# Optimization experiments

Measured on AMD Instinct MI355X. Metric: run time of the kernel, lower is better.

The kernel has to match this reference:

```python
import jax, jax.numpy as jnp
import numpy as np

N_BASIS = 8
CUTOFF = 5.0
NORM_FACTOR = 16.0


def setup_inputs() -> dict:
    key = jax.random.key(0)
    ks = jax.random.split(key, 10)
    N, E, C = 20000, 320000, 32
    s = 1.0 / np.sqrt(C)
    return {
        "node0": jax.random.normal(ks[0], (N, C), jnp.float32),
        "node1": jax.random.normal(ks[1], (N, C, 3), jnp.float32),
        "node2": jax.random.normal(ks[2], (N, C, 3, 3), jnp.float32),
        "rij": jax.random.normal(ks[3], (E, 3), jnp.float32) * 1.5,
        "Wrad": jax.random.normal(ks[4], (11, N_BASIS, C), jnp.float32) * 0.3,
        "U": jax.random.normal(ks[5], (3, C, C), jnp.float32) * s,
        "V": jax.random.normal(ks[6], (8, C, C), jnp.float32) * s,
        "Wg": jax.random.normal(ks[7], (3, C, C), jnp.float32) * s,
        "idx_i": jax.random.randint(ks[8], (E,), 0, N),
        "idx_j": jax.random.randint(ks[9], (E,), 0, N),
    }


def reference(node0, node1, node2, rij, Wrad, U, V, Wg, idx_i, idx_j):
    N, C = node0.shape
    # radial basis (Gaussian RBF * cosine cutoff envelope)
    dist = jnp.sqrt(jnp.sum(rij * rij, -1) + 1e-12)           # [E]
    rhat = rij / dist[:, None]                                 # [E,3]
    centers = jnp.linspace(0.5, CUTOFF, N_BASIS, dtype=node0.dtype)
    fc = 0.5 * (jnp.cos(jnp.pi * jnp.clip(dist / CUTOFF, 0.0, 1.0)) + 1.0)
    rbf = jnp.exp(-4.0 * (dist[:, None] - centers) ** 2) * fc[:, None]  # [E,B]
    # per-coupling-path radial filters: 11 paths (in_way, r_way, out_way)
    w = jnp.einsum('eb,pbc->pec', rbf, Wrad)                   # [11,E,C]
    # gather neighbor (node_j) features per edge
    g0 = node0[idx_j]                                          # [E,C]
    g1 = node1[idx_j]                                          # [E,C,3]
    g2 = node2[idx_j]                                          # [E,C,3,3]
    m1 = rhat                                                  # [E,3]
    m2 = rhat[:, :, None] * rhat[:, None, :]                   # [E,3,3]
    # graph conv: contract node_j tensor with r-way moment, weighted by radial filter
    # paths: 0:(0,0,0) 1:(0,1,1) 2:(0,2,2) 3:(1,0,1) 4:(1,1,0) 5:(1,1,2)
    #        6:(1,2,1) 7:(2,0,2) 8:(2,1,1) 9:(2,2,0) 10:(2,2,2)
    msg0 = (g0 * w[0]
            + jnp.einsum('eca,ea->ec', g1, m1) * w[4]
            + jnp.einsum('ecab,eab->ec', g2, m2) * w[9])
    msg1 = (jnp.einsum('ec,ea->eca', g0 * w[1], m1)
            + g1 * w[3][:, :, None]
            + jnp.einsum('eca,eab->ecb', g1, m2) * w[6][:, :, None]
            + jnp.einsum('ecab,eb->eca', g2, m1) * w[8][:, :, None])
    msg2 = (jnp.einsum('ec,eab->ecab', g0 * w[2], m2)
            + jnp.einsum('eca,eb->ecab', g1 * w[5][:, :, None], m1)
            + g2 * w[7][:, :, None, None]
            + jnp.einsum('ecab,ebd->ecad', g2, m2) * w[10][:, :, None, None])
    # scatter_add aggregation into per-atom features, normalized
    a0 = jax.ops.segment_sum(msg0, idx_i, num_segments=N) / NORM_FACTOR
    a1 = jax.ops.segment_sum(msg1, idx_i, num_segments=N) / NORM_FACTOR
    a2 = jax.ops.segment_sum(msg2, idx_i, num_segments=N) / NORM_FACTOR
    # multi-body self-interaction (2-body linear U + 3-body products V)
    y0 = (jnp.einsum('nc,cd->nd', a0, U[0])
          + jnp.einsum('nc,cd->nd', a0 * a0, V[0])
          + jnp.einsum('nc,cd->nd', jnp.einsum('nca,nca->nc', a1, a1), V[3])
          + jnp.einsum('nc,cd->nd', jnp.einsum('ncab,ncab->nc', a2, a2), V[6]))
    y1 = (jnp.einsum('nca,cd->nda', a1, U[1])
          + jnp.einsum('nca,cd->nda', a0[:, :, None] * a1, V[1])
          + jnp.einsum('nca,cd->nda', jnp.einsum('nca,ncab->ncb', a1, a2), V[5]))
    y2 = (jnp.einsum('ncab,cd->ndab', a2, U[2])
          + jnp.einsum('ncab,cd->ndab', a0[:, :, None, None] * a2, V[2])
          + jnp.einsum('ncab,cd->ndab', a1[:, :, :, None] * a1[:, :, None, :], V[4])
          + jnp.einsum('ncab,cd->ndab', jnp.einsum('ncab,ncbd->ncad', a2, a2), V[7]))
    # gated nonlinearity (scalar channel gates tensor ways) + residual add
    new0 = node0 + jax.nn.silu(y0 @ Wg[0])
    new1 = node1 + y1 * jax.nn.silu(y0 @ Wg[1])[:, :, None]
    new2 = node2 + y2 * jax.nn.silu(y0 @ Wg[2])[:, :, None, None]
    return (new0, new1, new2)
```

## Files before the change

kernel.cpp:

```cpp
#include <hip/hip_runtime.h>
#include <hip/hip_fp16.h>

#define NCH 32
#define NB 8
#define NPB 8

typedef __attribute__((ext_vector_type(2))) _Float16 half2r;

__device__ __forceinline__ unsigned short f2h(float f) {
    return __half_as_ushort(__float2half_rn(f));
}
__device__ __forceinline__ float h2f_lo(unsigned int u) {
    half2r v = __builtin_bit_cast(half2r, u);
    return (float)v.x;
}
__device__ __forceinline__ float h2f_hi(unsigned int u) {
    half2r v = __builtin_bit_cast(half2r, u);
    return (float)v.y;
}
__device__ __forceinline__ unsigned int pack2h(float lo, float hi) {
    return (unsigned int)f2h(lo) | ((unsigned int)f2h(hi) << 16);
}

__device__ __forceinline__ float fdot2u(unsigned int a, unsigned int b, float c) {
#if __has_builtin(__builtin_amdgcn_fdot2)
    return __builtin_amdgcn_fdot2(__builtin_bit_cast(half2r, a),
                                  __builtin_bit_cast(half2r, b), c, false);
#else
    half2r av = __builtin_bit_cast(half2r, a);
    half2r bv = __builtin_bit_cast(half2r, b);
    return c + (float)av.x * (float)bv.x + (float)av.y * (float)bv.y;
#endif
}

__device__ __forceinline__ void acc8h(float& y, uint4 w, uint4 f) {
    y = fdot2u(w.x, f.x, y);
    y = fdot2u(w.y, f.y, y);
    y = fdot2u(w.z, f.z, y);
    y = fdot2u(w.w, f.w, y);
}
__device__ __forceinline__ void acc8fh(float& y, uint4 w, float4 a, float4 b) {
    y += h2f_lo(w.x) * a.x + h2f_hi(w.x) * a.y + h2f_lo(w.y) * a.z + h2f_hi(w.y) * a.w
       + h2f_lo(w.z) * b.x + h2f_hi(w.z) * b.y + h2f_lo(w.w) * b.z + h2f_hi(w.w) * b.w;
}

__global__ __launch_bounds__(256) void wprep_kernel(
    const float* __restrict__ U, const float* __restrict__ V,
    const float* __restrict__ Wg, unsigned short* __restrict__ wswz)
{
    int idx = blockIdx.x * 256 + threadIdx.x;
    if (idx >= 14 * 1024) return;
    int m = idx >> 10, r = idx & 1023;
    int c = r >> 5, d = r & 31;
    float v;
    if (m < 3)       v = U[m * 1024 + c * 32 + d];
    else if (m < 11) v = V[(m - 3) * 1024 + c * 32 + d];
    else             v = Wg[(m - 11) * 1024 + c * 32 + d];
    wswz[m * 1024 + (c >> 3) * 256 + d * 8 + (c & 7)] = f2h(v);
}

__global__ __launch_bounds__(256) void wprep_rad_kernel(
    const float* __restrict__ Wrad, unsigned int* __restrict__ wradp)
{
    int idx = blockIdx.x * 256 + threadIdx.x;
    if (idx >= 11 * 4 * 32) return;
    int c = idx & 31, bb = (idx >> 5) & 3, p = idx >> 7;
    float lo = Wrad[p * 256 + (2 * bb) * 32 + c] * (1.0f / 16.0f);
    float hi = Wrad[p * 256 + (2 * bb + 1) * 32 + c] * (1.0f / 16.0f);
    wradp[c * 44 + p * 4 + bb] = pack2h(lo, hi);
}

__global__ __launch_bounds__(256) void hist_kernel(
    const int* __restrict__ idx_i, int* __restrict__ counts, int E)
{
    int e = blockIdx.x * 256 + threadIdx.x;
    if (e < E) atomicAdd(&counts[idx_i[e]], 1);
}

__global__ __launch_bounds__(256) void scan_reduce_kernel(
    const int* __restrict__ counts, int* __restrict__ blocksums, int N)
{
    const int tid = threadIdx.x;
    const int base = blockIdx.x * 1024;
    int v = 0;
    #pragma unroll
    for (int k = 0; k < 4; ++k) {
        int i = base + tid * 4 + k;
        if (i < N) v += counts[i];
    }
    #pragma unroll
    for (int off = 1; off < 64; off <<= 1) v += __shfl_xor(v, off, 64);
    __shared__ int wsum[4];
    if ((tid & 63) == 0) wsum[tid >> 6] = v;
    __syncthreads();
    if (tid == 0) blocksums[blockIdx.x] = wsum[0] + wsum[1] + wsum[2] + wsum[3];
}

__global__ void scan_top_kernel(
    const int* __restrict__ blocksums, int* __restrict__ bases,
    int* __restrict__ offsets, int nb, int N)
{
    int l = threadIdx.x;
    int v = (l < nb) ? blocksums[l] : 0;
    int incl = v;
    #pragma unroll
    for (int off = 1; off < 64; off <<= 1) {
        int t = __shfl_up(incl, off, 64);
        if (l >= off) incl += t;
    }
    if (l < nb) bases[l] = incl - v;
    if (l == nb - 1) offsets[N] = incl;
}

__global__ __launch_bounds__(256) void scan_write_kernel(
    int* __restrict__ cursor, const int* __restrict__ bases,
    int* __restrict__ offsets, int N)
{
    const int tid = threadIdx.x;
    const int i0 = blockIdx.x * 1024 + tid * 4;
    int v[4]; int lsum = 0;
    #pragma unroll
    for (int k = 0; k < 4; ++k) {
        int i = i0 + k;
        v[k] = (i < N) ? cursor[i] : 0;
        lsum += v[k];
    }
    int incl = lsum;
    #pragma unroll
    for (int off = 1; off < 64; off <<= 1) {
        int t = __shfl_up(incl, off, 64);
        if ((tid & 63) >= off) incl += t;
    }
    __shared__ int wsum[4];
    if ((tid & 63) == 63) wsum[tid >> 6] = incl;
    __syncthreads();
    int add = bases[blockIdx.x];
    for (int w = 0; w < (tid >> 6); ++w) add += wsum[w];
    int run = add + incl - lsum;
    #pragma unroll
    for (int k = 0; k < 4; ++k) {
        int i = i0 + k;
        if (i < N) { offsets[i] = run; cursor[i] = run; run += v[k]; }
    }
}

__global__ __launch_bounds__(256) void scatter_meta_kernel(
    const int* __restrict__ idx_i, const int* __restrict__ idx_j,
    const float* __restrict__ rij, int* __restrict__ cursor,
    int* __restrict__ jord, float4* __restrict__ meta2, int E)
{
    int e = blockIdx.x * 256 + threadIdx.x;
    if (e >= E) return;
    float rx = rij[3 * e + 0], ry = rij[3 * e + 1], rz = rij[3 * e + 2];
    float dist = sqrtf(rx * rx + ry * ry + rz * rz + 1e-12f);
    float inv = 1.0f / dist;
    float tcl = fminf(dist * 0.2f, 1.0f);
    float fc = 0.5f * (cosf(3.14159265358979f * tcl) + 1.0f);
    float rbf[NB];
    #pragma unroll
    for (int b = 0; b < NB; ++b) {
        float dd = dist - (0.5f + (float)b * (4.5f / 7.0f));
        rbf[b] = expf(-4.0f * dd * dd) * fc;
    }
    unsigned int rb01 = pack2h(rbf[0], rbf[1]);
    unsigned int rb23 = pack2h(rbf[2], rbf[3]);
    unsigned int rb45 = pack2h(rbf[4], rbf[5]);
    unsigned int rb67 = pack2h(rbf[6], rbf[7]);
    int slot = atomicAdd(&cursor[idx_i[e]], 1);
    jord[slot] = idx_j[e];
    meta2[2 * slot + 0] = make_float4(rx * inv, ry * inv, rz * inv, __uint_as_float(rb01));
    meta2[2 * slot + 1] = make_float4(__uint_as_float(rb23), __uint_as_float(rb45),
                                      __uint_as_float(rb67), 0.0f);
}

__global__ __launch_bounds__(256) void transpose_nodes_kernel(
    const float* __restrict__ node0, const float* __restrict__ node1,
    const float* __restrict__ node2, uint2* __restrict__ t0g,
    uint4* __restrict__ t1g, unsigned short* __restrict__ t2g, int N)
{
    __shared__ float s1[8 * 96];
    __shared__ float s2[8 * 288];
    const int nb0 = blockIdx.x * 8;
    const int remN = N - nb0;
    if (remN >= 8) {
        const float4* src1 = reinterpret_cast<const float4*>(node1 + (size_t)nb0 * 96);
        float4* d1 = reinterpret_cast<float4*>(s1);
        for (int i = threadIdx.x; i < 192; i += 256) d1[i] = src1[i];
        const float4* src2 = reinterpret_cast<const float4*>(node2 + (size_t)nb0 * 288);
        float4* d2 = reinterpret_cast<float4*>(s2);
        for (int i = threadIdx.x; i < 576; i += 256) d2[i] = src2[i];
    } else {
        const int tot1 = remN * 96;
        for (int i = threadIdx.x; i < 768; i += 256)
            s1[i] = (i < tot1) ? node1[(size_t)nb0 * 96 + i] : 0.f;
        const int tot2 = remN * 288;
        for (int i = threadIdx.x; i < 2304; i += 256)
            s2[i] = (i < tot2) ? node2[(size_t)nb0 * 288 + i] : 0.f;
    }
    __syncthreads();

    const int g = threadIdx.x >> 5;
    const int c = threadIdx.x & 31;
    const int n = nb0 + g;
    if (n >= N) return;

    float G0 = node0[(size_t)n * 32 + c];
    float G1[3];
    #pragma unroll
    for (int a = 0; a < 3; ++a) G1[a] = s1[g * 96 + c * 3 + a];
    float G2[9];
    #pragma unroll
    for (int k = 0; k < 9; ++k) G2[k] = s2[g * 288 + c * 9 + k];

    const size_t b = ((size_t)n << 5) + c;
    uint2 P0;
    P0.x = pack2h(G0, G1[0]);
    P0.y = pack2h(G1[1], G1[2]);
    uint4 P1;
    P1.x = pack2h(G2[0], G2[1]);
    P1.y = pack2h(G2[2], G2[3]);
    P1.z = pack2h(G2[4], G2[5]);
    P1.w = pack2h(G2[6], G2[7]);
    t0g[b] = P0;
    t1g[b] = P1;
    t2g[b] = f2h(G2[8]);
}

__device__ __forceinline__ void edge_compute(
    uint2 P0, uint4 P1, unsigned short g28, float4 M0, float4 M1,
    const uint4 wrq[11], float& A0, float (&A1)[3], float (&A2)[9])
{
    const float h0 = M0.x, h1 = M0.y, h2 = M0.z;
    const unsigned int rb01 = __float_as_uint(M0.w);
    const unsigned int rb23 = __float_as_uint(M1.x);
    const unsigned int rb45 = __float_as_uint(M1.y);
    const unsigned int rb67 = __float_as_uint(M1.z);

    float w[11];
    #pragma unroll
    for (int p = 0; p < 11; ++p)
        w[p] = fdot2u(rb01, wrq[p].x,
               fdot2u(rb23, wrq[p].y,
               fdot2u(rb45, wrq[p].z,
               fdot2u(rb67, wrq[p].w, 0.0f))));

    const float G0 = h2f_lo(P0.x);
    float G1[3];
    G1[0] = h2f_hi(P0.x); G1[1] = h2f_lo(P0.y); G1[2] = h2f_hi(P0.y);
    float G2[9];
    G2[0] = h2f_lo(P1.x); G2[1] = h2f_hi(P1.x);
    G2[2] = h2f_lo(P1.y); G2[3] = h2f_hi(P1.y);
    G2[4] = h2f_lo(P1.z); G2[5] = h2f_hi(P1.z);
    G2[6] = h2f_lo(P1.w); G2[7] = h2f_hi(P1.w);
    G2[8] = __half2float(__ushort_as_half(g28));

    const float hh[3] = {h0, h1, h2};
    const float s1 = G1[0] * h0 + G1[1] * h1 + G1[2] * h2;
    float tt[3];
    #pragma unroll
    for (int a = 0; a < 3; ++a)
        tt[a] = G2[a * 3 + 0] * h0 + G2[a * 3 + 1] * h1 + G2[a * 3 + 2] * h2;
    const float s2 = tt[0] * h0 + tt[1] * h1 + tt[2] * h2;

    A0 += G0 * w[0] + s1 * w[4] + s2 * w[9];
    #pragma unroll
    for (int a = 0; a < 3; ++a)
        A1[a] += (G0 * w[1] + s1 * w[6]) * hh[a] + G1[a] * w[3] + tt[a] * w[8];
    #pragma unroll
    for (int a = 0; a < 3; ++a) {
        float pre = G0 * w[2] * hh[a] + G1[a] * w[5] + tt[a] * w[10];
        #pragma unroll
        for (int b = 0; b < 3; ++b)
            A2[a * 3 + b] += pre * hh[b] + G2[a * 3 + b] * w[7];
    }
}

__global__ __launch_bounds__(256) void aggregate_kernel(
    const uint2* __restrict__ t0g, const uint4* __restrict__ t1g,
    const unsigned short* __restrict__ t2g, const unsigned int* __restrict__ wradp,
    const int* __restrict__ jord, const float4* __restrict__ meta2,
    const int* __restrict__ offsets,
    float* __restrict__ a0, float* __restrict__ a1, float* __restrict__ a2,
    int N)
{
    const int lane = threadIdx.x & 63;
    const int c = lane & 31;
    const int side = lane >> 5;
    const int n = blockIdx.x * 4 + (threadIdx.x >> 6);
    if (n >= N) return;

    uint4 wrq[11];
    {
        const uint4* wrv = reinterpret_cast<const uint4*>(wradp) + c * 11;
        #pragma unroll
        for (int p = 0; p < 11; ++p) wrq[p] = wrv[p];
    }

    const int beg = offsets[n], end = offsets[n + 1];
    const int deg = end - beg;

    float A0 = 0.f;
    float A1[3] = {0.f, 0.f, 0.f};
    float A2[9] = {0.f, 0.f, 0.f, 0.f, 0.f, 0.f, 0.f, 0.f, 0.f};

    if (deg > 0) {
        const int last = end - 1;
        int eA = beg + side;
        int eB = eA + 2;
        int jA2 = jord[min(eA + 4, last)];
        int jB2 = jord[min(eB + 4, last)];

        uint2 P0A, P0B; uint4 P1A, P1B; unsigned short s2A, s2B;
        float4 M0A, M1A, M0B, M1B;
        {
            const int jA = jord[min(eA, last)];
            const size_t b = ((size_t)jA << 5) + c;
            P0A = t0g[b]; P1A = t1g[b]; s2A = t2g[b];
            const int em = min(eA, last);
            M0A = meta2[2 * em]; M1A = meta2[2 * em + 1];
        }
        {
            const int jB = jord[min(eB, last)];
            const size_t b = ((size_t)jB << 5) + c;
            P0B = t0g[b]; P1B = t1g[b]; s2B = t2g[b];
            const int em = min(eB, last);
            M0B = meta2[2 * em]; M1B = meta2[2 * em + 1];
        }

        const int M = (deg + 3) >> 2;

#define SLOT_STEP(P0s, P1s, s2s, M0s, M1s, eS, jS2)                         \
        {                                                                   \
            const uint2 P0 = P0s; const uint4 P1 = P1s;                     \
            const unsigned short g28 = s2s;                                 \
            const float4 Mm0 = M0s, Mm1 = M1s;                              \
            const bool v = (eS < end);                                      \
            const int eSn = eS + 4;                                         \
            {                                                               \
                const size_t b = ((size_t)jS2 << 5) + c;                    \
                P0s = t0g[b]; P1s = t1g[b]; s2s = t2g[b];                   \
                const int em = min(eSn, last);                              \
                M0s = meta2[2 * em]; M1s = meta2[2 * em + 1];               \
            }                                                               \
            jS2 = jord[min(eSn + 4, last)];                                 \
            if (v) edge_compute(P0, P1, g28, Mm0, Mm1, wrq, A0, A1, A2);    \
            eS = eSn;                                                       \
        }

        for (int m = 0; m < M; ++m) {
            SLOT_STEP(P0A, P1A, s2A, M0A, M1A, eA, jA2)
            SLOT_STEP(P0B, P1B, s2B, M0B, M1B, eB, jB2)
        }
#undef SLOT_STEP
    }

    A0 += __shfl_xor(A0, 32, 64);
    #pragma unroll
    for (int a = 0; a < 3; ++a) A1[a] += __shfl_xor(A1[a], 32, 64);
    #pragma unroll
    for (int k = 0; k < 9; ++k) A2[k] += __shfl_xor(A2[k], 32, 64);

    if (side == 0) {
        a0[n * 32 + c] = A0;
        #pragma unroll
        for (int a = 0; a < 3; ++a) a1[n * 96 + a * 32 + c] = A1[a];
        #pragma unroll
        for (int k = 0; k < 9; ++k) a2[n * 288 + k * 32 + c] = A2[k];
    }
}

__global__ __launch_bounds__(256) void node_kernel(
    const float* __restrict__ node0, const float* __restrict__ node1,
    const float* __restrict__ node2, const unsigned short* __restrict__ wswz,
    float* __restrict__ out0, float* __restrict__ out1, float* __restrict__ out2,
    int N)
{
    __shared__ alignas(16) unsigned short wT[14 * 1024];
    __shared__ alignas(16) unsigned short feat[NPB * 49 * 32];
    __shared__ alignas(16) float y0s[NPB][32];

    {
        const uint4* src = reinterpret_cast<const uint4*>(wswz);
        uint4* dst = reinterpret_cast<uint4*>(wT);
        for (int i = threadIdx.x; i < 14 * 128; i += 256) dst[i] = src[i];
    }

    const int g = threadIdx.x >> 5;
    const int lane = threadIdx.x & 31;
    const int n = blockIdx.x * NPB + g;
    const bool active = (n < N);

    if (active) {
        const int c = lane;
        float A0 = out0[n * 32 + c];
        float A1[3], A2[9];
        #pragma unroll
        for (int a = 0; a < 3; ++a) A1[a] = out1[n * 96 + a * 32 + c];
        #pragma unroll
        for (int k = 0; k < 9; ++k) A2[k] = out2[n * 288 + k * 32 + c];

        unsigned short* F = &feat[g * 49 * 32];
        F[0 * 32 + c] = f2h(A0);
        F[1 * 32 + c] = f2h(A0 * A0);
        F[2 * 32 + c] = f2h(A1[0] * A1[0] + A1[1] * A1[1] + A1[2] * A1[2]);
        float n2 = 0.f;
        #pragma unroll
        for (int k = 0; k < 9; ++k) n2 += A2[k] * A2[k];
        F[3 * 32 + c] = f2h(n2);
        #pragma unroll
        for (int a = 0; a < 3; ++a) {
            F[(4 + a) * 32 + c] = f2h(A1[a]);
            F[(7 + a) * 32 + c] = f2h(A0 * A1[a]);
        }
        #pragma unroll
        for (int b = 0; b < 3; ++b) {
            float s = A1[0] * A2[0 * 3 + b] + A1[1] * A2[1 * 3 + b] + A1[2] * A2[2 * 3 + b];
            F[(10 + b) * 32 + c] = f2h(s);
        }
        #pragma unroll
        for (int k = 0; k < 9; ++k) {
            F[(13 + k) * 32 + c] = f2h(A2[k]);
            F[(22 + k) * 32 + c] = f2h(A0 * A2[k]);
        }
        #pragma unroll
        for (int a = 0; a < 3; ++a)
            #pragma unroll
            for (int b = 0; b < 3; ++b)
                F[(31 + a * 3 + b) * 32 + c] = f2h(A1[a] * A1[b]);
        #pragma unroll
        for (int a = 0; a < 3; ++a)
            #pragma unroll
            for (int dd = 0; dd < 3; ++dd) {
                float s = A2[a * 3 + 0] * A2[0 * 3 + dd] + A2[a * 3 + 1] * A2[1 * 3 + dd]
                        + A2[a * 3 + 2] * A2[2 * 3 + dd];
                F[(40 + a * 3 + dd) * 32 + c] = f2h(s);
            }
    }
    __syncthreads();

    const int d = lane;
    float y0v = 0.f;
    float y1v[3] = {0.f, 0.f, 0.f};
    float y2v[9] = {0.f, 0.f, 0.f, 0.f, 0.f, 0.f, 0.f, 0.f, 0.f};

    if (active) {
        const uint4* W4 = reinterpret_cast<const uint4*>(wT);
        const uint4* F4 = reinterpret_cast<const uint4*>(&feat[g * 49 * 32]);
        for (int q = 0; q < 4; ++q) {
            const int q32d = q * 32 + d;
            acc8h(y0v, W4[0 * 128 + q32d], F4[0 * 4 + q]);
            acc8h(y0v, W4[3 * 128 + q32d], F4[1 * 4 + q]);
            acc8h(y0v, W4[6 * 128 + q32d], F4[2 * 4 + q]);
            acc8h(y0v, W4[9 * 128 + q32d], F4[3 * 4 + q]);
            uint4 wU1 = W4[1 * 128 + q32d];
            uint4 wV1 = W4[4 * 128 + q32d];
            uint4 wV5 = W4[8 * 128 + q32d];
            #pragma unroll
            for (int a = 0; a < 3; ++a) {
                acc8h(y1v[a], wU1, F4[(4 + a) * 4 + q]);
                acc8h(y1v[a], wV1, F4[(7 + a) * 4 + q]);
                acc8h(y1v[a], wV5, F4[(10 + a) * 4 + q]);
            }
            uint4 wU2 = W4[2 * 128 + q32d];
            uint4 wV2 = W4[5 * 128 + q32d];
            uint4 wV4 = W4[7 * 128 + q32d];
            uint4 wV7 = W4[10 * 128 + q32d];
            #pragma unroll
            for (int k = 0; k < 9; ++k) {
                acc8h(y2v[k], wU2, F4[(13 + k) * 4 + q]);
                acc8h(y2v[k], wV2, F4[(22 + k) * 4 + q]);
                acc8h(y2v[k], wV4, F4[(31 + k) * 4 + q]);
                acc8h(y2v[k], wV7, F4[(40 + k) * 4 + q]);
            }
        }
        y0s[g][d] = y0v;
    }
    __syncthreads();

    if (!active) return;

    float t0 = 0.f, t1 = 0.f, t2 = 0.f;
    {
        const uint4* W4 = reinterpret_cast<const uint4*>(wT);
        const float4* Y4 = reinterpret_cast<const float4*>(y0s[g]);
        #pragma unroll
        for (int q = 0; q < 4; ++q) {
            const int q32d = q * 32 + d;
            float4 ya = Y4[2 * q], yb = Y4[2 * q + 1];
            acc8fh(t0, W4[11 * 128 + q32d], ya, yb);
            acc8fh(t1, W4[12 * 128 + q32d], ya, yb);
            acc8fh(t2, W4[13 * 128 + q32d], ya, yb);
        }
    }
    float s0 = t0 / (1.0f + expf(-t0));
    float s1 = t1 / (1.0f + expf(-t1));
    float s2 = t2 / (1.0f + expf(-t2));

    out0[n * 32 + d] = node0[n * 32 + d] + s0;
    #pragma unroll
    for (int a = 0; a < 3; ++a)
        out1[n * 96 + d * 3 + a] = node1[n * 96 + d * 3 + a] + y1v[a] * s1;
    #pragma unroll
    for (int k = 0; k < 9; ++k)
        out2[n * 288 + d * 9 + k] = node2[n * 288 + d * 9 + k] + y2v[k] * s2;
}

extern "C" void kernel_launch(void* const* d_in, const int* in_sizes, int n_in,
                              void* d_out, int out_size, void* d_ws, size_t ws_size,
                              hipStream_t stream)
{
    const float* node0 = (const float*)d_in[0];
    const float* node1 = (const float*)d_in[1];
    const float* node2 = (const float*)d_in[2];
    const float* rij   = (const float*)d_in[3];
    const float* Wrad  = (const float*)d_in[4];
    const float* U     = (const float*)d_in[5];
    const float* V     = (const float*)d_in[6];
    const float* Wg    = (const float*)d_in[7];
    const int* idx_i   = (const int*)d_in[8];
    const int* idx_j   = (const int*)d_in[9];

    const int N = in_sizes[0] / 32;
    const int E = in_sizes[3] / 3;

    float* out0 = (float*)d_out;
    float* out1 = out0 + (size_t)N * 32;
    float* out2 = out1 + (size_t)N * 96;

    size_t off = 0;
    auto walloc = [&](size_t bytes) -> void* {
        off = (off + 63) & ~(size_t)63;
        void* p = (char*)d_ws + off;
        off += bytes;
        return p;
    };
    int*    cursor    = (int*)   walloc((size_t)N * 4);
    int*    offsets   = (int*)   walloc((size_t)(N + 1) * 4);
    int*    blocksums = (int*)   walloc(64 * 4);
    int*    bases     = (int*)   walloc(64 * 4);
    int*    jord      = (int*)   walloc((size_t)E * 4);
    float4* meta2     = (float4*)walloc((size_t)E * 2 * sizeof(float4));
    uint2*  t0g       = (uint2*) walloc((size_t)N * 32 * sizeof(uint2));
    uint4*  t1g       = (uint4*) walloc((size_t)N * 32 * sizeof(uint4));
    unsigned short* t2g = (unsigned short*)walloc((size_t)N * 32 * 2);
    unsigned short* wswz = (unsigned short*)walloc(14 * 1024 * 2);
    unsigned int*  wradp = (unsigned int*)walloc(11 * 4 * 32 * 4);
    (void)ws_size;

    const int nb = (N + 1023) / 1024;

    hipMemsetAsync(cursor, 0, (size_t)N * sizeof(int), stream);

    wprep_kernel<<<dim3(56), dim3(256), 0, stream>>>(U, V, Wg, wswz);
    wprep_rad_kernel<<<dim3(6), dim3(256), 0, stream>>>(Wrad, wradp);
    hist_kernel<<<dim3((E + 255) / 256), dim3(256), 0, stream>>>(idx_i, cursor, E);
    scan_reduce_kernel<<<dim3(nb), dim3(256), 0, stream>>>(cursor, blocksums, N);
    scan_top_kernel<<<dim3(1), dim3(64), 0, stream>>>(blocksums, bases, offsets, nb, N);
    scan_write_kernel<<<dim3(nb), dim3(256), 0, stream>>>(cursor, bases, offsets, N);
    scatter_meta_kernel<<<dim3((E + 255) / 256), dim3(256), 0, stream>>>(
        idx_i, idx_j, rij, cursor, jord, meta2, E);
    transpose_nodes_kernel<<<dim3((N + 7) / 8), dim3(256), 0, stream>>>(
        node0, node1, node2, t0g, t1g, t2g, N);

    aggregate_kernel<<<dim3((N + 3) / 4), dim3(256), 0, stream>>>(
        t0g, t1g, t2g, wradp, jord, meta2, offsets, out0, out1, out2, N);

    node_kernel<<<dim3((N + NPB - 1) / NPB), dim3(256), 0, stream>>>(
        node0, node1, node2, wswz, out0, out1, out2, N);
}
```

Before: 271.6 us.

## Balance aggregation across 8-node edge ranges with shared-memory atomic accumulation

The aggregate kernel used to give each node its own wavefront, which leaves lanes idle when node degrees differ. Now each block takes 8 nodes and spreads their combined CSR edge range over 8 warps. Each edge carries its local node index (i & 7) in the spare meta slot and adds its 13 message components into shared-memory accumulators through atomics, split by side to reduce conflicts. The gain is load balance across degree variation, at the cost of 13 LDS float atomics per edge per channel plus extra syncs and LDS use.

New measurement: 922.6 us. 3.4x slower.

```diff
diff --git a/kernel.cpp b/kernel.cpp
--- a/kernel.cpp
+++ b/kernel.cpp
@@ -166,11 +166,13 @@
     unsigned int rb23 = pack2h(rbf[2], rbf[3]);
     unsigned int rb45 = pack2h(rbf[4], rbf[5]);
     unsigned int rb67 = pack2h(rbf[6], rbf[7]);
-    int slot = atomicAdd(&cursor[idx_i[e]], 1);
+    const int i = idx_i[e];
+    int slot = atomicAdd(&cursor[i], 1);
     jord[slot] = idx_j[e];
     meta2[2 * slot + 0] = make_float4(rx * inv, ry * inv, rz * inv, __uint_as_float(rb01));
     meta2[2 * slot + 1] = make_float4(__uint_as_float(rb23), __uint_as_float(rb45),
-                                      __uint_as_float(rb67), 0.0f);
+                                      __uint_as_float(rb67),
+                                      __uint_as_float((unsigned int)(i & 7)));
 }
 
 __global__ __launch_bounds__(256) void transpose_nodes_kernel(
@@ -226,15 +228,16 @@
     t2g[b] = f2h(G2[8]);
 }
 
-__device__ __forceinline__ void edge_compute(
+__device__ __forceinline__ void edge_accum(
     uint2 P0, uint4 P1, unsigned short g28, float4 M0, float4 M1,
-    const uint4 wrq[11], float& A0, float (&A1)[3], float (&A2)[9])
+    const uint4 wrq[11], float* __restrict__ accSide, int c)
 {
     const float h0 = M0.x, h1 = M0.y, h2 = M0.z;
     const unsigned int rb01 = __float_as_uint(M0.w);
     const unsigned int rb23 = __float_as_uint(M1.x);
     const unsigned int rb45 = __float_as_uint(M1.y);
     const unsigned int rb67 = __float_as_uint(M1.z);
+    const int nloc = (int)__float_as_uint(M1.w);
 
     float w[11];
     #pragma unroll
@@ -262,16 +265,35 @@
         tt[a] = G2[a * 3 + 0] * h0 + G2[a * 3 + 1] * h1 + G2[a * 3 + 2] * h2;
     const float s2 = tt[0] * h0 + tt[1] * h1 + tt[2] * h2;
 
-    A0 += G0 * w[0] + s1 * w[4] + s2 * w[9];
-    #pragma unroll
-    for (int a = 0; a < 3; ++a)
-        A1[a] += (G0 * w[1] + s1 * w[6]) * hh[a] + G1[a] * w[3] + tt[a] * w[8];
+    float* base = accSide + nloc * (13 * 32) + c;
+
+    float m0 = G0 * w[0];
+    m0 = fmaf(s1, w[4], m0);
+    m0 = fmaf(s2, w[9], m0);
+    atomicAdd(base + 0 * 32, m0);
+
+    float t01 = G0 * w[1];
+    t01 = fmaf(s1, w[6], t01);
     #pragma unroll
     for (int a = 0; a < 3; ++a) {
-        float pre = G0 * w[2] * hh[a] + G1[a] * w[5] + tt[a] * w[10];
-        #pragma unroll
-        for (int b = 0; b < 3; ++b)
-            A2[a * 3 + b] += pre * hh[b] + G2[a * 3 + b] * w[7];
+        float u = t01 * hh[a];
+        u = fmaf(G1[a], w[3], u);
+        u = fmaf(tt[a], w[8], u);
+        atomicAdd(base + (1 + a) * 32, u);
+    }
+
+    const float g0w2 = G0 * w[2];
+    #pragma unroll
+    for (int a = 0; a < 3; ++a) {
+        float pre = g0w2 * hh[a];
+        pre = fmaf(G1[a], w[5], pre);
+        pre = fmaf(tt[a], w[10], pre);
+        #pragma unroll
+        for (int b = 0; b < 3; ++b) {
+            float u = pre * hh[b];
+            u = fmaf(G2[a * 3 + b], w[7], u);
+            atomicAdd(base + (4 + a * 3 + b) * 32, u);
+        }
     }
 }
 
@@ -283,11 +305,14 @@
     float* __restrict__ a0, float* __restrict__ a1, float* __restrict__ a2,
     int N)
 {
-    const int lane = threadIdx.x & 63;
-    const int c = lane & 31;
-    const int side = lane >> 5;
-    const int n = blockIdx.x * 4 + (threadIdx.x >> 6);
-    if (n >= N) return;
+    __shared__ float acc[2 * 8 * 13 * 32];
+
+    const int tid = threadIdx.x;
+    const int c = tid & 31;
+    const int side = (tid >> 5) & 1;
+    const int g = tid >> 5;
+
+    for (int i = tid; i < 2 * 8 * 13 * 32; i += 256) acc[i] = 0.f;
 
     uint4 wrq[11];
     {
@@ -296,76 +321,79 @@
         for (int p = 0; p < 11; ++p) wrq[p] = wrv[p];
     }
 
-    const int beg = offsets[n], end = offsets[n + 1];
-    const int deg = end - beg;
-
-    float A0 = 0.f;
-    float A1[3] = {0.f, 0.f, 0.f};
-    float A2[9] = {0.f, 0.f, 0.f, 0.f, 0.f, 0.f, 0.f, 0.f, 0.f};
-
-    if (deg > 0) {
-        const int last = end - 1;
-        int eA = beg + side;
-        int eB = eA + 2;
-        int jA2 = jord[min(eA + 4, last)];
-        int jB2 = jord[min(eB + 4, last)];
-
+    const int n0 = blockIdx.x * NPB;
+    const int ebeg = offsets[n0];
+    const int eend = offsets[min(n0 + NPB, N)];
+    const int ne = eend - ebeg;
+
+    float* accSide = acc + side * (8 * 13 * 32);
+
+    __syncthreads();
+
+    if (ne > 0) {
+        const int elast = eend - 1;
+        int eA = ebeg + g;
+        int eB = eA + 8;
         uint2 P0A, P0B; uint4 P1A, P1B; unsigned short s2A, s2B;
         float4 M0A, M1A, M0B, M1B;
         {
-            const int jA = jord[min(eA, last)];
-            const size_t b = ((size_t)jA << 5) + c;
+            const int em = min(eA, elast);
+            const int j = jord[em];
+            const size_t b = ((size_t)j << 5) + c;
             P0A = t0g[b]; P1A = t1g[b]; s2A = t2g[b];
-            const int em = min(eA, last);
             M0A = meta2[2 * em]; M1A = meta2[2 * em + 1];
         }
         {
-            const int jB = jord[min(eB, last)];
-            const size_t b = ((size_t)jB << 5) + c;
+            const int em = min(eB, elast);
+            const int j = jord[em];
+            const size_t b = ((size_t)j << 5) + c;
             P0B = t0g[b]; P1B = t1g[b]; s2B = t2g[b];
-            const int em = min(eB, last);
             M0B = meta2[2 * em]; M1B = meta2[2 * em + 1];
         }
-
-        const int M = (deg + 3) >> 2;
+        int jA2 = jord[min(eA + 16, elast)];
+        int jB2 = jord[min(eB + 16, elast)];
+
+        const int T = (ne + 15) >> 4;
 
 #define SLOT_STEP(P0s, P1s, s2s, M0s, M1s, eS, jS2)                         \
         {                                                                   \
             const uint2 P0 = P0s; const uint4 P1 = P1s;                     \
             const unsigned short g28 = s2s;                                 \
             const float4 Mm0 = M0s, Mm1 = M1s;                              \
-            const bool v = (eS < end);                                      \
-            const int eSn = eS + 4;                                         \
+            const bool v = (eS < eend);                                     \
+            const int eSn = eS + 16;                                        \
             {                                                               \
                 const size_t b = ((size_t)jS2 << 5) + c;                    \
                 P0s = t0g[b]; P1s = t1g[b]; s2s = t2g[b];                   \
-                const int em = min(eSn, last);                              \
+                const int em = min(eSn, elast);                             \
                 M0s = meta2[2 * em]; M1s = meta2[2 * em + 1];               \
             }                                                               \
-            jS2 = jord[min(eSn + 4, last)];                                 \
-            if (v) edge_compute(P0, P1, g28, Mm0, Mm1, wrq, A0, A1, A2);    \
+            jS2 = jord[min(eSn + 16, elast)];                               \
+            if (v) edge_accum(P0, P1, g28, Mm0, Mm1, wrq, accSide, c);      \
             eS = eSn;                                                       \
         }
 
-        for (int m = 0; m < M; ++m) {
+        for (int t = 0; t < T; ++t) {
             SLOT_STEP(P0A, P1A, s2A, M0A, M1A, eA, jA2)
             SLOT_STEP(P0B, P1B, s2B, M0B, M1B, eB, jB2)
         }
 #undef SLOT_STEP
     }
 
-    A0 += __shfl_xor(A0, 32, 64);
-    #pragma unroll
-    for (int a = 0; a < 3; ++a) A1[a] += __shfl_xor(A1[a], 32, 64);
-    #pragma unroll
-    for (int k = 0; k < 9; ++k) A2[k] += __shfl_xor(A2[k], 32, 64);
-
-    if (side == 0) {
-        a0[n * 32 + c] = A0;
-        #pragma unroll
-        for (int a = 0; a < 3; ++a) a1[n * 96 + a * 32 + c] = A1[a];
-        #pragma unroll
-        for (int k = 0; k < 9; ++k) a2[n * 288 + k * 32 + c] = A2[k];
+    __syncthreads();
+
+    for (int i = tid; i < 8 * 13 * 32; i += 256) {
+        const float v = acc[i] + acc[8 * 13 * 32 + i];
+        const int nloc = i / (13 * 32);
+        const int r = i - nloc * (13 * 32);
+        const int comp = r >> 5;
+        const int cc = r & 31;
+        const int n = n0 + nloc;
+        if (n < N) {
+            if (comp == 0)      a0[n * 32 + cc] = v;
+            else if (comp < 4)  a1[n * 96 + (comp - 1) * 32 + cc] = v;
+            else                a2[n * 288 + (comp - 4) * 32 + cc] = v;
+        }
     }
 }
 
@@ -562,7 +590,7 @@
     transpose_nodes_kernel<<<dim3((N + 7) / 8), dim3(256), 0, stream>>>(
         node0, node1, node2, t0g, t1g, t2g, N);
 
-    aggregate_kernel<<<dim3((N + 3) / 4), dim3(256), 0, stream>>>(
+    aggregate_kernel<<<dim3((N + NPB - 1) / NPB), dim3(256), 0, stream>>>(
         t0g, t1g, t2g, wradp, jord, meta2, offsets, out0, out1, out2, N);
 
     node_kernel<<<dim3((N + NPB - 1) / NPB), dim3(256), 0, stream>>>(
```
